# Kernel optimization log

Hardware: AMD Instinct MI355X
Metric: run time of the kernel (lower is better)

Reference implementation:

```python
import jax, jax.numpy as jnp
import numpy as np

T, B, DIM = 1024, 32, 1024
H, N = 8, 64
INIT_BETA_BIAS = 2.0
EPS = 1e-6


def setup_inputs() -> dict:
    key = jax.random.key(0)
    ks = jax.random.split(key, 5)
    scale = 1.0 / np.sqrt(DIM)  # xavier-ish
    return {
        "x": jax.random.normal(ks[0], (T, B, DIM), dtype=jnp.float32),
        "W_k": jax.random.normal(ks[1], (H * N, DIM), dtype=jnp.float32) * scale,
        "W_v": jax.random.normal(ks[2], (H * N, DIM), dtype=jnp.float32) * scale,
        "W_q": jax.random.normal(ks[3], (H * N, DIM), dtype=jnp.float32) * scale,
        "W_beta": jax.random.normal(ks[4], (H * N, DIM), dtype=jnp.float32) * scale,
        "b_beta": jnp.full((H, N), INIT_BETA_BIAS, dtype=jnp.float32),
    }


def reference(x, W_k, W_v, W_q, W_beta, b_beta):
    Tn, Bn, D = x.shape
    Hn, n = b_beta.shape
    xf = x.reshape(Tn * Bn, D)
    k_all = (xf @ W_k.T).reshape(Tn, Bn, Hn, n)
    v_all = (xf @ W_v.T).reshape(Tn, Bn, Hn, n)
    q_all = (xf @ W_q.T).reshape(Tn, Bn, Hn, n)
    beta_all = jax.nn.sigmoid((xf @ W_beta.T).reshape(Tn, Bn, Hn, n) + b_beta)
    k_norm = k_all / (jnp.linalg.norm(k_all, axis=-1, keepdims=True) + EPS)

    def step(S, inp):
        k, v, q, beta = inp  # each [B, H, n]
        retrieved = jnp.einsum('bhij,bhj->bhi', S, k)
        delta = v - retrieved
        outer = jnp.einsum('bhi,bhj->bhij', delta, k)
        S = jnp.tanh(beta[..., None] * S + outer)
        Sq = jnp.einsum('bhij,bhj->bhi', S, q)
        out = Sq * jax.nn.silu(Sq)  # [B, H, n]
        return S, out.reshape(Bn, Hn * n)

    S0 = jnp.zeros((Bn, Hn, n, n), dtype=x.dtype)
    S_final, output = jax.lax.scan(step, S0, (k_norm, v_all, q_all, beta_all))
    return output, S_final  # output: [T, B, H*n]
```

## Files before the change

### kernel.cpp

```cpp
#include <hip/hip_runtime.h>
#include <stdint.h>

#define TSTEPS 1024
#define BATCH  32
#define DIMK   1024
#define HEADS  8
#define NHEAD  64
#define NPROJ  2048
#define MROWS  (TSTEPS*BATCH)

typedef _Float16 f16;
typedef _Float16 f16x2 __attribute__((ext_vector_type(2)));
typedef _Float16 f16x4 __attribute__((ext_vector_type(4)));
typedef _Float16 f16x8 __attribute__((ext_vector_type(8)));
typedef float    f32x4 __attribute__((ext_vector_type(4)));
typedef unsigned int u32;

#define AS_GLOBAL __attribute__((address_space(1)))
#define AS_LDS    __attribute__((address_space(3)))

__device__ __forceinline__ void load_lds_16B(const void* g, void* l){
  __builtin_amdgcn_global_load_lds((const AS_GLOBAL u32*)g, (AS_LDS u32*)l, 16, 0, 0);
}

__device__ __forceinline__ float sigmoid_fast(float x){
  return __builtin_amdgcn_rcpf(1.0f + __expf(-x));
}
__device__ __forceinline__ float tanh_fast(float x){
  float e = __expf(2.0f*x);
  return fmaf(-2.0f, __builtin_amdgcn_rcpf(e + 1.0f), 1.0f);
}

__device__ __forceinline__ float fdot2(f16x2 a, f16x2 b, float c){
#if __has_builtin(__builtin_amdgcn_fdot2)
  typedef __fp16 h16x2 __attribute__((ext_vector_type(2)));
  return __builtin_amdgcn_fdot2(__builtin_bit_cast(h16x2, a),
                                __builtin_bit_cast(h16x2, b), c, false);
#else
  return fmaf((float)a[1], (float)b[1], fmaf((float)a[0], (float)b[0], c));
#endif
}

__device__ __forceinline__ f16x2 pack2(float a, float b){
#if __has_builtin(__builtin_amdgcn_cvt_pkrtz)
  return __builtin_bit_cast(f16x2, __builtin_amdgcn_cvt_pkrtz(a, b));
#else
  f16x2 r = { (f16)a, (f16)b };
  return r;
#endif
}

__global__ __launch_bounds__(256) void cast_kernel(const float4* __restrict__ src,
                                                   f16x4* __restrict__ dst, int n4){
  int i = blockIdx.x*blockDim.x + threadIdx.x;
  int stride = gridDim.x*blockDim.x;
  for (; i < n4; i += stride){
    float4 v = src[i];
    f16x4 o = { (f16)v.x, (f16)v.y, (f16)v.z, (f16)v.w };
    dst[i] = o;
  }
}

#define BM 128
#define BN 128
#define BK 32

__global__ __launch_bounds__(256) void gemm_xwT(const f16* __restrict__ A,
                                                const f16* __restrict__ B,
                                                f16* __restrict__ C){
  __shared__ f16 sA[BM*BK];
  __shared__ f16 sB[BN*BK];
  const int t = threadIdx.x;
  const int w = t >> 6;
  const int l = t & 63;
  const int bm = blockIdx.x;
  const int bn = blockIdx.y;
  const int wr = w >> 1, wc = w & 1;

  f32x4 acc[4][4] = {};

  const int srow = t >> 2;
  const int scol = (t & 3) * 8;
  const f16* gA0 = A + (size_t)(bm*BM + srow)*DIMK + scol;
  const f16* gB0 = B + (size_t)(bn*BN + srow)*DIMK + scol;
  char* sAb = (char*)sA;
  char* sBb = (char*)sB;
  const int ldsw = w*1024;

  for (int kk = 0; kk < DIMK/BK; ++kk){
    const f16* pa = gA0 + kk*BK;
    const f16* pb = gB0 + kk*BK;
    load_lds_16B(pa,           sAb + ldsw);
    load_lds_16B(pa + 64*DIMK, sAb + ldsw + 4096);
    load_lds_16B(pb,           sBb + ldsw);
    load_lds_16B(pb + 64*DIMK, sBb + ldsw + 4096);
    __syncthreads();

    f16x8 af[4], bf[4];
    #pragma unroll
    for (int mi=0; mi<4; ++mi){
      int arow = wr*64 + mi*16 + (l & 15);
      af[mi] = *(const f16x8*)(sAb + arow*64 + (l>>4)*16);
    }
    #pragma unroll
    for (int ni=0; ni<4; ++ni){
      int brow = wc*64 + ni*16 + (l & 15);
      bf[ni] = *(const f16x8*)(sBb + brow*64 + (l>>4)*16);
    }
    #pragma unroll
    for (int mi=0; mi<4; ++mi)
      #pragma unroll
      for (int ni=0; ni<4; ++ni)
        acc[mi][ni] = __builtin_amdgcn_mfma_f32_16x16x32_f16(af[mi], bf[ni], acc[mi][ni], 0, 0, 0);
    __syncthreads();
  }

  const int crow0 = bm*BM + wr*64 + (l>>4)*4;
  const int ccol0 = bn*BN + wc*64 + (l & 15);
  #pragma unroll
  for (int mi=0; mi<4; ++mi)
    #pragma unroll
    for (int ni=0; ni<4; ++ni)
      #pragma unroll
      for (int r=0; r<4; ++r)
        C[(size_t)(crow0 + mi*16 + r)*NPROJ + ccol0 + ni*16] = (f16)acc[mi][ni][r];
}

__global__ __launch_bounds__(256) void prep_kernel(f16* __restrict__ Y,
                                                   const float* __restrict__ b_beta){
  int g = blockIdx.x*4 + (threadIdx.x >> 6);
  int l = threadIdx.x & 63;
  int h = g & 7;
  f16* y = Y + (size_t)(g >> 3)*NPROJ + h*NHEAD + l;
  float k  = (float)y[0];
  float br = (float)y[1536];
  float ss = k*k;
  #pragma unroll
  for (int d=1; d<64; d<<=1) ss += __shfl_xor(ss, d);
  y[0]    = (f16)(k * __builtin_amdgcn_rcpf(__builtin_sqrtf(ss) + 1e-6f));
  y[1536] = (f16)sigmoid_fast(br + b_beta[h*NHEAD + l]);
}

struct Stage { f16x2 kl, kh, ql, qh; float v, bb; };

__device__ __forceinline__ Stage load_stage(const f16* base, int tn, int cb, int row){
  const f16* pn = base + (size_t)tn * (BATCH*NPROJ);
  Stage s;
  uint2 ku = *(const uint2*)(pn + cb);
  uint2 qu = *(const uint2*)(pn + 1024 + cb);
  s.kl = __builtin_bit_cast(f16x2, ku.x);
  s.kh = __builtin_bit_cast(f16x2, ku.y);
  s.ql = __builtin_bit_cast(f16x2, qu.x);
  s.qh = __builtin_bit_cast(f16x2, qu.y);
  s.v  = (float)pn[512 + row];
  s.bb = (float)pn[1536 + row];
  return s;
}

__device__ __forceinline__ void step_compute(const Stage& st, int tt, int g,
                                             float& S0, float& S1, float& S2, float& S3,
                                             f16x2& P0, f16x2& P1,
                                             float* outp){
  float kf0 = (float)st.kl[0], kf1 = (float)st.kl[1];
  float kf2 = (float)st.kh[0], kf3 = (float)st.kh[1];

  float r = fdot2(P0, st.kl, 0.f);
  r = fdot2(P1, st.kh, r);
  r += __shfl_xor(r, 1);
  r += __shfl_xor(r, 2);
  r += __shfl_xor(r, 4);
  r += __shfl_xor(r, 8);
  float delta = st.v - r;

  float a0 = tanh_fast(fmaf(st.bb, S0, delta*kf0));
  float a1 = tanh_fast(fmaf(st.bb, S1, delta*kf1));
  float a2 = tanh_fast(fmaf(st.bb, S2, delta*kf2));
  float a3 = tanh_fast(fmaf(st.bb, S3, delta*kf3));
  S0=a0; S1=a1; S2=a2; S3=a3;
  P0 = pack2(a0, a1);
  P1 = pack2(a2, a3);

  float sq = fdot2(P0, st.ql, 0.f);
  sq = fdot2(P1, st.qh, sq);
  sq += __shfl_xor(sq, 1);
  sq += __shfl_xor(sq, 2);
  sq += __shfl_xor(sq, 4);
  sq += __shfl_xor(sq, 8);
  float sg = sigmoid_fast(sq);
  float o  = sq*sq*sg;
  if (g == 0) outp[(size_t)tt * (BATCH*512)] = o;
}

__global__ __launch_bounds__(1024) void scan_kernel(const f16* __restrict__ Y,
                                                    float* __restrict__ out,
                                                    float* __restrict__ S_out){
  const int p = blockIdx.x;
  const int b = p >> 3, h = p & 7;
  const int t = threadIdx.x;
  const int row = t >> 4;
  const int g   = t & 15;
  const int cb  = g*4;

  float S0=0.f, S1=0.f, S2=0.f, S3=0.f;
  f16x2 P0 = {}, P1 = {};

  const f16* base = Y + (size_t)b*NPROJ + h*NHEAD;
  float* outp = out + (size_t)b*512 + h*NHEAD + row;

  Stage sA = load_stage(base, 0, cb, row);
  Stage sB = load_stage(base, 1, cb, row);
  Stage sC, sD;

  #pragma unroll 1
  for (int tt=0; tt<TSTEPS; tt+=4){
    sC = load_stage(base, tt+2, cb, row);
    step_compute(sA, tt,   g, S0,S1,S2,S3, P0,P1, outp);
    sD = load_stage(base, tt+3, cb, row);
    step_compute(sB, tt+1, g, S0,S1,S2,S3, P0,P1, outp);
    sA = load_stage(base, tt+4, cb, row);
    step_compute(sC, tt+2, g, S0,S1,S2,S3, P0,P1, outp);
    sB = load_stage(base, tt+5, cb, row);
    step_compute(sD, tt+3, g, S0,S1,S2,S3, P0,P1, outp);
  }

  size_t sbase = ((size_t)p*NHEAD + row)*NHEAD + cb;
  float4 v4 = { S0, S1, S2, S3 };
  *(float4*)(S_out + sbase) = v4;
}

extern "C" void kernel_launch(void* const* d_in, const int* in_sizes, int n_in,
                              void* d_out, int out_size, void* d_ws, size_t ws_size,
                              hipStream_t stream){
  const float* x  = (const float*)d_in[0];
  const float* Wk = (const float*)d_in[1];
  const float* Wv = (const float*)d_in[2];
  const float* Wq = (const float*)d_in[3];
  const float* Wb = (const float*)d_in[4];
  const float* bb = (const float*)d_in[5];

  float* out = (float*)d_out;
  float* Sf  = out + (size_t)TSTEPS*BATCH*512;

  char* ws = (char*)d_ws;
  f16* xh = (f16*)ws;
  f16* wh = (f16*)(ws + 67108864);
  f16* Yh = (f16*)(ws + 67108864 + 4194304);

  cast_kernel<<<2048, 256, 0, stream>>>((const float4*)x,  (f16x4*)xh, (MROWS*DIMK)/4);
  cast_kernel<<<512,  256, 0, stream>>>((const float4*)Wk, (f16x4*)(wh + 0*524288), 524288/4);
  cast_kernel<<<512,  256, 0, stream>>>((const float4*)Wv, (f16x4*)(wh + 1*524288), 524288/4);
  cast_kernel<<<512,  256, 0, stream>>>((const float4*)Wq, (f16x4*)(wh + 2*524288), 524288/4);
  cast_kernel<<<512,  256, 0, stream>>>((const float4*)Wb, (f16x4*)(wh + 3*524288), 524288/4);

  dim3 g(MROWS/BM, NPROJ/BN);
  gemm_xwT<<<g, 256, 0, stream>>>(xh, wh, Yh);

  prep_kernel<<<(TSTEPS*BATCH*HEADS)/4, 256, 0, stream>>>(Yh, bb);

  scan_kernel<<<256, 1024, 0, stream>>>(Yh, out, Sf);
}
```

Measured before the change: 873.5 us.

## Shorten scan critical path: prescaled exp2 tanh, packed math, deferred SiLU

The beta gate is prescaled by 2*log2(e) in the prep kernel, and the delta term gets the same scale, so tanh uses a raw exp2 with no multiply. The state update is written as packed float2 arithmetic so the compiler can emit packed FMA instructions. The sigmoid-based output activation is removed from the serial scan loop and applied by a new elementwise kernel afterwards. This moves work off the latency-bound recurrence, at the cost of an extra launch and a read-modify-write pass over the output; storing the scaled beta in fp16 slightly changes rounding.

Measured after the change: 800.2 us. -8.4%, faster.

```diff
diff --git a/kernel.cpp b/kernel.cpp
--- a/kernel.cpp
+++ b/kernel.cpp
@@ -13,12 +13,15 @@
 typedef _Float16 f16x2 __attribute__((ext_vector_type(2)));
 typedef _Float16 f16x4 __attribute__((ext_vector_type(4)));
 typedef _Float16 f16x8 __attribute__((ext_vector_type(8)));
+typedef float    f32x2 __attribute__((ext_vector_type(2)));
 typedef float    f32x4 __attribute__((ext_vector_type(4)));
 typedef unsigned int u32;
 
 #define AS_GLOBAL __attribute__((address_space(1)))
 #define AS_LDS    __attribute__((address_space(3)))
 
+#define C2LOG2E 2.8853900817779268f
+
 __device__ __forceinline__ void load_lds_16B(const void* g, void* l){
   __builtin_amdgcn_global_load_lds((const AS_GLOBAL u32*)g, (AS_LDS u32*)l, 16, 0, 0);
 }
@@ -26,9 +29,13 @@
 __device__ __forceinline__ float sigmoid_fast(float x){
   return __builtin_amdgcn_rcpf(1.0f + __expf(-x));
 }
-__device__ __forceinline__ float tanh_fast(float x){
-  float e = __expf(2.0f*x);
-  return fmaf(-2.0f, __builtin_amdgcn_rcpf(e + 1.0f), 1.0f);
+
+__device__ __forceinline__ float exp2_fast(float x){
+#if __has_builtin(__builtin_amdgcn_exp2f)
+  return __builtin_amdgcn_exp2f(x);
+#else
+  return __expf(0.6931471805599453f * x);
+#endif
 }
 
 __device__ __forceinline__ float fdot2(f16x2 a, f16x2 b, float c){
@@ -138,7 +145,7 @@
   #pragma unroll
   for (int d=1; d<64; d<<=1) ss += __shfl_xor(ss, d);
   y[0]    = (f16)(k * __builtin_amdgcn_rcpf(__builtin_sqrtf(ss) + 1e-6f));
-  y[1536] = (f16)sigmoid_fast(br + b_beta[h*NHEAD + l]);
+  y[1536] = (f16)(C2LOG2E * sigmoid_fast(br + b_beta[h*NHEAD + l]));
 }
 
 struct Stage { f16x2 kl, kh, ql, qh; float v, bb; };
@@ -158,37 +165,41 @@
 }
 
 __device__ __forceinline__ void step_compute(const Stage& st, int tt, int g,
-                                             float& S0, float& S1, float& S2, float& S3,
+                                             f32x2& S01, f32x2& S23,
                                              f16x2& P0, f16x2& P1,
                                              float* outp){
-  float kf0 = (float)st.kl[0], kf1 = (float)st.kl[1];
-  float kf2 = (float)st.kh[0], kf3 = (float)st.kh[1];
-
-  float r = fdot2(P0, st.kl, 0.f);
-  r = fdot2(P1, st.kh, r);
+  float r = fdot2(P1, st.kh, fdot2(P0, st.kl, 0.f));
   r += __shfl_xor(r, 1);
   r += __shfl_xor(r, 2);
   r += __shfl_xor(r, 4);
   r += __shfl_xor(r, 8);
-  float delta = st.v - r;
-
-  float a0 = tanh_fast(fmaf(st.bb, S0, delta*kf0));
-  float a1 = tanh_fast(fmaf(st.bb, S1, delta*kf1));
-  float a2 = tanh_fast(fmaf(st.bb, S2, delta*kf2));
-  float a3 = tanh_fast(fmaf(st.bb, S3, delta*kf3));
-  S0=a0; S1=a1; S2=a2; S3=a3;
-  P0 = pack2(a0, a1);
-  P1 = pack2(a2, a3);
-
-  float sq = fdot2(P0, st.ql, 0.f);
-  sq = fdot2(P1, st.qh, sq);
+  float dl = (st.v - r) * C2LOG2E;
+
+  f32x2 d2  = { dl, dl };
+  f32x2 bb2 = { st.bb, st.bb };
+  f32x2 k01 = { (float)st.kl[0], (float)st.kl[1] };
+  f32x2 k23 = { (float)st.kh[0], (float)st.kh[1] };
+  f32x2 arg01 = bb2*S01 + d2*k01;
+  f32x2 arg23 = bb2*S23 + d2*k23;
+
+  f32x2 e01 = { exp2_fast(arg01.x), exp2_fast(arg01.y) };
+  f32x2 e23 = { exp2_fast(arg23.x), exp2_fast(arg23.y) };
+  f32x2 one2 = { 1.f, 1.f };
+  e01 += one2;  e23 += one2;
+  f32x2 t01 = { __builtin_amdgcn_rcpf(e01.x), __builtin_amdgcn_rcpf(e01.y) };
+  f32x2 t23 = { __builtin_amdgcn_rcpf(e23.x), __builtin_amdgcn_rcpf(e23.y) };
+  f32x2 m2 = { -2.f, -2.f };
+  S01 = m2*t01 + one2;
+  S23 = m2*t23 + one2;
+  P0 = pack2(S01.x, S01.y);
+  P1 = pack2(S23.x, S23.y);
+
+  float sq = fdot2(P1, st.qh, fdot2(P0, st.ql, 0.f));
   sq += __shfl_xor(sq, 1);
   sq += __shfl_xor(sq, 2);
   sq += __shfl_xor(sq, 4);
   sq += __shfl_xor(sq, 8);
-  float sg = sigmoid_fast(sq);
-  float o  = sq*sq*sg;
-  if (g == 0) outp[(size_t)tt * (BATCH*512)] = o;
+  if (g == 0) outp[(size_t)tt * (BATCH*512)] = sq;
 }
 
 __global__ __launch_bounds__(1024) void scan_kernel(const f16* __restrict__ Y,
@@ -201,7 +212,7 @@
   const int g   = t & 15;
   const int cb  = g*4;
 
-  float S0=0.f, S1=0.f, S2=0.f, S3=0.f;
+  f32x2 S01 = {0.f, 0.f}, S23 = {0.f, 0.f};
   f16x2 P0 = {}, P1 = {};
 
   const f16* base = Y + (size_t)b*NPROJ + h*NHEAD;
@@ -214,18 +225,31 @@
   #pragma unroll 1
   for (int tt=0; tt<TSTEPS; tt+=4){
     sC = load_stage(base, tt+2, cb, row);
-    step_compute(sA, tt,   g, S0,S1,S2,S3, P0,P1, outp);
+    step_compute(sA, tt,   g, S01,S23, P0,P1, outp);
     sD = load_stage(base, tt+3, cb, row);
-    step_compute(sB, tt+1, g, S0,S1,S2,S3, P0,P1, outp);
+    step_compute(sB, tt+1, g, S01,S23, P0,P1, outp);
     sA = load_stage(base, tt+4, cb, row);
-    step_compute(sC, tt+2, g, S0,S1,S2,S3, P0,P1, outp);
+    step_compute(sC, tt+2, g, S01,S23, P0,P1, outp);
     sB = load_stage(base, tt+5, cb, row);
-    step_compute(sD, tt+3, g, S0,S1,S2,S3, P0,P1, outp);
+    step_compute(sD, tt+3, g, S01,S23, P0,P1, outp);
   }
 
   size_t sbase = ((size_t)p*NHEAD + row)*NHEAD + cb;
-  float4 v4 = { S0, S1, S2, S3 };
+  float4 v4 = { S01.x, S01.y, S23.x, S23.y };
   *(float4*)(S_out + sbase) = v4;
+}
+
+__global__ __launch_bounds__(256) void silu_kernel(float4* __restrict__ o, int n4){
+  int i = blockIdx.x*blockDim.x + threadIdx.x;
+  int stride = gridDim.x*blockDim.x;
+  for (; i < n4; i += stride){
+    float4 v = o[i];
+    v.x = v.x*v.x*sigmoid_fast(v.x);
+    v.y = v.y*v.y*sigmoid_fast(v.y);
+    v.z = v.z*v.z*sigmoid_fast(v.z);
+    v.w = v.w*v.w*sigmoid_fast(v.w);
+    o[i] = v;
+  }
 }
 
 extern "C" void kernel_launch(void* const* d_in, const int* in_sizes, int n_in,
@@ -258,4 +282,6 @@
   prep_kernel<<<(TSTEPS*BATCH*HEADS)/4, 256, 0, stream>>>(Yh, bb);
 
   scan_kernel<<<256, 1024, 0, stream>>>(Yh, out, Sf);
-}
+
+  silu_kernel<<<2048, 256, 0, stream>>>((float4*)out, (TSTEPS*BATCH*512)/4);
+}
```
